# Kernel optimization log

Measured on AMD Instinct MI355X. Metric: run time of the kernel, lower is better.

The kernel has to match this reference:

```python
import jax, jax.numpy as jnp
import numpy as np

B, N, L = 32, 1024, 128
K, D_E, H = 3, 16, 4


def setup_inputs() -> dict:
    key = jax.random.key(0)
    ks = jax.random.split(key, 7)
    return {
        "x": jax.random.normal(ks[0], (B, N, L), jnp.float32),
        # mild scaling on embeddings/projections keeps softmax logits in a sane range
        "psi_emb": jax.random.normal(ks[1], (N, D_E), jnp.float32) * 0.3,
        "psi": jnp.float32(1.0),
        "W_q": jax.random.normal(ks[2], (D_E, H, D_E), jnp.float32) * 0.2,
        "W_k": jax.random.normal(ks[3], (D_E, H, D_E), jnp.float32) * 0.2,
        "attn_alpha": jnp.float32(0.5),
        "F_w": jax.random.normal(ks[4], (H, D_E, K + 1, L), jnp.float32) * 0.1,
        "f_b": jax.random.normal(ks[5], (H, D_E), jnp.float32),
        "head_mix": jnp.ones((H,), jnp.float32),
    }


def reference(x, psi_emb, psi, W_q, W_k, attn_alpha, F_w, f_b, head_mix):
    # x: (B, N, L)
    n = x.shape[1]
    # --- gaussian adjacency: softmax over columns of exp(-psi * ||psi_i - psi_j||^2)
    diff = psi_emb[:, None, :] - psi_emb[None, :, :]          # (N, N, d_e)
    dist2 = jnp.sum(diff * diff, axis=-1)                     # (N, N)
    A_base = jax.nn.softmax(jnp.exp(-psi * dist2), axis=1)    # (N, N)
    # --- per-head attention adjacency
    Q = jnp.einsum('nd,dhm->nhm', psi_emb, W_q)               # (N, H, d_e)
    Kt = jnp.einsum('nd,dhm->nhm', psi_emb, W_k)              # (N, H, d_e)
    scale = 1.0 / jnp.sqrt(jnp.asarray(Q.shape[-1], x.dtype))
    A_attn = jax.nn.softmax(
        jnp.einsum('nhd,mhd->hnm', Q, Kt) * scale, axis=-1)   # (H, N, N)
    # --- sigmoid blend (all heads at once)
    alpha = jax.nn.sigmoid(attn_alpha)
    A_eff = alpha * A_base[None] + (1.0 - alpha) * A_attn     # (H, N, N)
    # --- Chebyshev recursion: T0 = I, T1 = A, Tk = 2 A T_{k-1} - T_{k-2}
    I = jnp.broadcast_to(jnp.eye(n, dtype=x.dtype), A_eff.shape)
    supports = [I, A_eff]
    for _ in range(2, K + 1):
        supports.append(2.0 * jnp.einsum('hnm,hml->hnl', A_eff, supports[-1]) - supports[-2])
    S = jnp.stack(supports, axis=1)                           # (H, K+1, N, N)
    # --- per-node filters
    W_filter = jnp.einsum('nd,hdkl->hnkl', psi_emb, F_w)      # (H, N, K+1, L)
    b_filter = jnp.einsum('nd,hd->hn', psi_emb, f_b)          # (H, N)
    # --- graph conv + node-specific contraction
    x_g = jnp.einsum('hknm,bml->bhknl', S, x)                 # (B, H, K+1, N, L)
    out_h = jnp.einsum('bhknl,hnkl->bhn', x_g, W_filter) + b_filter[None]
    # --- head mixing
    mix_w = jax.nn.softmax(head_mix, axis=0)                  # (H,)
    return jnp.einsum('bhn,h->bn', out_h, mix_w)              # (B, N)
```

## Files before the change

### kernel.cpp

```cpp
#include <hip/hip_runtime.h>
#include <cstdint>

#define NN 1024
#define BB 32
#define LL 128
#define DE 16
#define HH 4
#define K1 4
#define BD 512
#define NS 524288

using bf16x8 = __attribute__((ext_vector_type(8))) short;
using f32x4  = __attribute__((ext_vector_type(4))) float;
using u16x4  = __attribute__((ext_vector_type(4))) unsigned short;

__device__ inline unsigned short f2bf(float f) {
    unsigned u = __builtin_bit_cast(unsigned, f);
    u += 0x7FFFu + ((u >> 16) & 1u);
    return (unsigned short)(u >> 16);
}
__device__ inline float bf2f(unsigned short u) {
    return __builtin_bit_cast(float, (unsigned)u << 16);
}

typedef const __attribute__((address_space(1))) void gas_void;
typedef __attribute__((address_space(3))) void las_void;
#define GLD16(gsrc, ldst) \
    __builtin_amdgcn_global_load_lds((gas_void*)(gsrc), (las_void*)(ldst), 16, 0, 0)

struct LogitsSmem {
    float ejs[64][17];
    float eis[64][17];
    float kjs[64][64];
    float qis[4][64][17];
    float part[4][5][64];
    float wq[1024];
    float wk[1024];
};
struct XtSmem { float xs[64][128]; };

__global__ __launch_bounds__(256) void phase1(
    const float* __restrict__ psi_emb, const float* __restrict__ psi_p,
    const float* __restrict__ W_q, const float* __restrict__ W_k,
    const float* __restrict__ x, const float* __restrict__ F_w,
    short* __restrict__ bnt, short* __restrict__ ant, float* __restrict__ partials,
    short* __restrict__ xt, short* __restrict__ wtt, float* __restrict__ out)
{
    __shared__ __align__(16) char smem_raw[sizeof(LogitsSmem)];
    const int bid = blockIdx.x;
    const int tid = threadIdx.x;

    if (bid < 256) {
        LogitsSmem& S = *(LogitsSmem*)smem_raw;
        const int jb = bid & 15, ib = bid >> 4;
        const int i0 = ib * 64, j0 = jb * 64;
        {
            const int row = tid >> 2, dq = (tid & 3) * 4;
            const float4 vj = *(const float4*)(psi_emb + (j0 + row) * DE + dq);
            S.ejs[row][dq] = vj.x; S.ejs[row][dq + 1] = vj.y;
            S.ejs[row][dq + 2] = vj.z; S.ejs[row][dq + 3] = vj.w;
            const float4 vi = *(const float4*)(psi_emb + (i0 + row) * DE + dq);
            S.eis[row][dq] = vi.x; S.eis[row][dq + 1] = vi.y;
            S.eis[row][dq + 2] = vi.z; S.eis[row][dq + 3] = vi.w;
            *(float4*)&S.wq[tid * 4] = *(const float4*)(W_q + tid * 4);
            *(float4*)&S.wk[tid * 4] = *(const float4*)(W_k + tid * 4);
        }
        __syncthreads();
#pragma unroll
        for (int rep = 0; rep < 16; rep++) {
            const int idx = rep * 256 + tid;
            const int row = idx >> 6, hm = idx & 63;
            float qv = 0.f, kv = 0.f;
#pragma unroll
            for (int d = 0; d < DE; d++) {
                qv += S.eis[row][d] * S.wq[d * 64 + hm];
                kv += S.ejs[row][d] * S.wk[d * 64 + hm];
            }
            S.qis[hm >> 4][row][hm & 15] = qv;
            S.kjs[row][hm] = kv;
        }
        __syncthreads();

        const int i = tid & 63, jg = tid >> 6;
        const float psi = psi_p[0];
        float er[DE];
#pragma unroll
        for (int d = 0; d < DE; d++) er[d] = S.eis[i][d];

        float sb = 0.f, sa[HH] = {0.f, 0.f, 0.f, 0.f};
#pragma unroll
        for (int g = 0; g < 2; g++) {
            unsigned short bw[8];
#pragma unroll
            for (int r = 0; r < 8; r++) {
                const int j = jg * 16 + g * 8 + r;
                float d2 = 0.f;
#pragma unroll
                for (int d = 0; d < DE; d++) { const float t = er[d] - S.ejs[j][d]; d2 += t * t; }
                const float bn = __expf(__expf(-psi * d2));
                sb += bn;
                bw[r] = f2bf(bn);
            }
            uint4 pk;
            pk.x = bw[0] | ((unsigned)bw[1] << 16);
            pk.y = bw[2] | ((unsigned)bw[3] << 16);
            pk.z = bw[4] | ((unsigned)bw[5] << 16);
            pk.w = bw[6] | ((unsigned)bw[7] << 16);
            const size_t toff = (size_t)((j0 + jg * 16 + g * 8) >> 3) * 8192 + (size_t)(i0 + i) * 8;
            *(uint4*)(bnt + toff) = pk;
        }
#pragma unroll
        for (int h = 0; h < HH; h++) {
            float qr[DE];
#pragma unroll
            for (int m = 0; m < DE; m++) qr[m] = S.qis[h][i][m];
#pragma unroll
            for (int g = 0; g < 2; g++) {
                unsigned short aw[8];
#pragma unroll
                for (int r = 0; r < 8; r++) {
                    const int j = jg * 16 + g * 8 + r;
                    float dot = 0.f;
#pragma unroll
                    for (int m = 0; m < DE; m++) dot += qr[m] * S.kjs[j][h * DE + m];
                    const float an = __expf(dot * 0.25f);
                    sa[h] += an;
                    aw[r] = f2bf(an);
                }
                uint4 pk;
                pk.x = aw[0] | ((unsigned)aw[1] << 16);
                pk.y = aw[2] | ((unsigned)aw[3] << 16);
                pk.z = aw[4] | ((unsigned)aw[5] << 16);
                pk.w = aw[6] | ((unsigned)aw[7] << 16);
                const size_t toff = (size_t)((j0 + jg * 16 + g * 8) >> 3) * 8192 + (size_t)(i0 + i) * 8;
                *(uint4*)(ant + (size_t)h * 1048576 + toff) = pk;
            }
        }
        S.part[jg][0][i] = sb;
#pragma unroll
        for (int h = 0; h < HH; h++) S.part[jg][1 + h][i] = sa[h];
        __syncthreads();
        if (tid < 64) {
#pragma unroll
            for (int s = 0; s < 5; s++) {
                const float v = S.part[0][s][tid] + S.part[1][s][tid] +
                                S.part[2][s][tid] + S.part[3][s][tid];
                partials[(size_t)jb * 5120 + (size_t)s * 1024 + i0 + tid] = v;
            }
        }
    } else if (bid < 768) {
        XtSmem& X = *(XtSmem*)smem_raw;
        const int idx = bid - 256;
        const int m0 = (idx & 15) * 64;
        const int b  = idx >> 4;
        for (int i = tid; i < 2048; i += 256) {
            const int row = i >> 5, lq = i & 31;
            *(float4*)&X.xs[row][lq * 4] =
                *(const float4*)(x + ((size_t)(b * NN + m0 + row)) * LL + lq * 4);
        }
        __syncthreads();
        for (int j = tid; j < 1024; j += 256) {
            const int m = j & 63, lc = j >> 6;
            const float* s = &X.xs[m][lc * 8];
            uint4 pk;
            pk.x = f2bf(s[0]) | ((unsigned)f2bf(s[1]) << 16);
            pk.y = f2bf(s[2]) | ((unsigned)f2bf(s[3]) << 16);
            pk.z = f2bf(s[4]) | ((unsigned)f2bf(s[5]) << 16);
            pk.w = f2bf(s[6]) | ((unsigned)f2bf(s[7]) << 16);
            *(uint4*)(xt + (size_t)b * 131072 + (size_t)lc * 8192 + (size_t)(m0 + m) * 8) = pk;
        }
    } else if (bid < 784) {
        const int j = (bid - 768) * 256 + tid;
        const int lc = j >> 8, c = j & 255;
        const int h = c >> 6, k = (c >> 4) & 3, d = c & 15;
        const float* s = F_w + (size_t)((h * DE + d) * K1 + k) * LL + lc * 8;
        uint4 pk;
        pk.x = f2bf(s[0]) | ((unsigned)f2bf(s[1]) << 16);
        pk.y = f2bf(s[2]) | ((unsigned)f2bf(s[3]) << 16);
        pk.z = f2bf(s[4]) | ((unsigned)f2bf(s[5]) << 16);
        pk.w = f2bf(s[6]) | ((unsigned)f2bf(s[7]) << 16);
        *(uint4*)(wtt + (size_t)lc * 2048 + (size_t)c * 8) = pk;
    } else {
        const int idx = (bid - 784) * 256 + tid;
        const float4 z = {0.f, 0.f, 0.f, 0.f};
        *(float4*)(out + (size_t)idx * 8) = z;
        *(float4*)(out + (size_t)idx * 8 + 4) = z;
    }
}

__global__ __launch_bounds__(256) void phase2(
    const short* __restrict__ xt, const short* __restrict__ wtt,
    short* __restrict__ Gt,
    const short* __restrict__ bnt, const short* __restrict__ ant,
    const float* __restrict__ partials, const float* __restrict__ alpha_p,
    short* __restrict__ At)
{
    const int bid = blockIdx.x;
    const int tid = threadIdx.x;
    __shared__ float sums_l[5][64];

    if (bid < 1024) {
        const int cb = bid & 3;
        const int m0 = ((bid >> 2) & 15) * 64;
        const int bp = bid >> 6;
        const int wave = tid >> 6, lane = tid & 63;
        const int b  = bp * 2 + (wave >> 1);
        const int wc = wave & 1;
        const int q = lane >> 4, m16 = lane & 15;
        const short* xb = xt + (size_t)b * 131072;

        f32x4 acc[4][2];
#pragma unroll
        for (int mi = 0; mi < 4; mi++)
#pragma unroll
            for (int ni = 0; ni < 2; ni++) acc[mi][ni] = (f32x4){0.f, 0.f, 0.f, 0.f};

#pragma unroll
        for (int ks = 0; ks < 4; ks++) {
            const int kc = ks * 4 + q;
            bf16x8 a[4], bb[2];
#pragma unroll
            for (int mi = 0; mi < 4; mi++)
                a[mi] = *(const bf16x8*)(xb + (size_t)kc * 8192 + (size_t)(m0 + mi * 16 + m16) * 8);
#pragma unroll
            for (int ni = 0; ni < 2; ni++)
                bb[ni] = *(const bf16x8*)(wtt + (size_t)kc * 2048 +
                                          (size_t)(cb * 64 + wc * 32 + ni * 16 + m16) * 8);
#pragma unroll
            for (int mi = 0; mi < 4; mi++)
#pragma unroll
                for (int ni = 0; ni < 2; ni++)
                    acc[mi][ni] = __builtin_amdgcn_mfma_f32_16x16x32_bf16(a[mi], bb[ni], acc[mi][ni], 0, 0, 0);
        }

#pragma unroll
        for (int ni = 0; ni < 2; ni++) {
            const int cc = cb * 64 + wc * 32 + ni * 16 + m16;
            const int kk = (cc >> 4) & 3, hh = cc >> 6;
            const int col512 = b * 16 + (cc & 15);
            short* gdst = Gt + (size_t)(kk * 4 + hh) * 524288;
#pragma unroll
            for (int mi = 0; mi < 4; mi++) {
                const int row0 = m0 + mi * 16 + q * 4;
                ushort4 pk;
                pk.x = f2bf(acc[mi][ni][0]); pk.y = f2bf(acc[mi][ni][1]);
                pk.z = f2bf(acc[mi][ni][2]); pk.w = f2bf(acc[mi][ni][3]);
                *(ushort4*)(gdst + ((size_t)(row0 >> 3) * 512 + col512) * 8 + (row0 & 7)) = pk;
            }
        }
    } else {
        const int idx = bid - 1024;
        const int jb = idx & 15, ib = idx >> 4;
        const int i0 = ib * 64, j0 = jb * 64;
        const int lane = tid & 63, w = tid >> 6;
        {
            float acc = 0.f;
#pragma unroll
            for (int jb2 = 0; jb2 < 16; jb2++)
                acc += partials[(size_t)jb2 * 5120 + (size_t)w * 1024 + i0 + lane];
            sums_l[w][lane] = acc;
            if (w == 0) {
                float a4 = 0.f;
#pragma unroll
                for (int jb2 = 0; jb2 < 16; jb2++)
                    a4 += partials[(size_t)jb2 * 5120 + 4 * 1024 + i0 + lane];
                sums_l[4][lane] = a4;
            }
        }
        __syncthreads();
        const int i = lane, jg = w;
        const float alpha = 1.f / (1.f + __expf(-alpha_p[0]));
        const float ibs = alpha / sums_l[0][i];
        float ias[HH];
#pragma unroll
        for (int h = 0; h < HH; h++) ias[h] = (1.f - alpha) / sums_l[1 + h][i];

#pragma unroll
        for (int g = 0; g < 2; g++) {
            const size_t toff = (size_t)((j0 + jg * 16 + g * 8) >> 3) * 8192 + (size_t)(i0 + i) * 8;
            const uint4 bp = *(const uint4*)(bnt + toff);
            float bnv[8];
            bnv[0] = bf2f(bp.x & 0xFFFF); bnv[1] = bf2f(bp.x >> 16);
            bnv[2] = bf2f(bp.y & 0xFFFF); bnv[3] = bf2f(bp.y >> 16);
            bnv[4] = bf2f(bp.z & 0xFFFF); bnv[5] = bf2f(bp.z >> 16);
            bnv[6] = bf2f(bp.w & 0xFFFF); bnv[7] = bf2f(bp.w >> 16);
#pragma unroll
            for (int h = 0; h < HH; h++) {
                const uint4 ap = *(const uint4*)(ant + (size_t)h * 1048576 + toff);
                float av[8];
                av[0] = bf2f(ap.x & 0xFFFF); av[1] = bf2f(ap.x >> 16);
                av[2] = bf2f(ap.y & 0xFFFF); av[3] = bf2f(ap.y >> 16);
                av[4] = bf2f(ap.z & 0xFFFF); av[5] = bf2f(ap.z >> 16);
                av[6] = bf2f(ap.w & 0xFFFF); av[7] = bf2f(ap.w >> 16);
                unsigned short ow[8];
#pragma unroll
                for (int r = 0; r < 8; r++) ow[r] = f2bf(ibs * bnv[r] + ias[h] * av[r]);
                uint4 pk;
                pk.x = ow[0] | ((unsigned)ow[1] << 16);
                pk.y = ow[2] | ((unsigned)ow[3] << 16);
                pk.z = ow[4] | ((unsigned)ow[5] << 16);
                pk.w = ow[6] | ((unsigned)ow[7] << 16);
                *(uint4*)(At + (size_t)h * 1048576 + toff) = pk;
            }
        }
    }
}

__global__ __launch_bounds__(256) void gemm_mf(
    const short* __restrict__ At, const short* __restrict__ Bt,
    const short* __restrict__ Pt, const short* __restrict__ Qt,
    short* __restrict__ Ot, float scale, float pc, float qc)
{
    const int bid = blockIdx.x;
    const int h = (bid & 7) >> 1;
    const int tile = ((bid >> 3) << 1) | (bid & 1);
    const int c0 = (tile & 7) * 64;
    const int r0 = (tile >> 3) * 64;

    const short* Ah = At + (size_t)h * 1048576;
    const short* Bh = Bt + (size_t)h * 524288;
    const short* Ph = Pt + (size_t)h * 524288;
    const short* Qh = Qt + (size_t)h * 524288;
    short* Oh = Ot + (size_t)h * 524288;

    const int tid = threadIdx.x;
    const int wave = tid >> 6, lane = tid & 63;
    const int q = lane >> 4, m16 = lane & 15;
    const int wr = wave >> 1, wc = wave & 1;

    __shared__ __align__(16) short Asm[4][4][64][8];
    __shared__ __align__(16) short Bsm[4][4][64][8];

    const char* Abase = (const char*)Ah + (size_t)r0 * 16;
    const char* Bbase = (const char*)Bh + (size_t)c0 * 16;

#define STAGE_MF(itc, bufc)                                                     \
    do {                                                                        \
        const size_t ko_ = (size_t)((itc) * 4 + wave);                          \
        GLD16(Abase + ko_ * 16384 + (size_t)lane * 16, &Asm[bufc][wave][0][0]); \
        GLD16(Bbase + ko_ * 8192  + (size_t)lane * 16, &Bsm[bufc][wave][0][0]); \
    } while (0)

    f32x4 acc[2][2];
#pragma unroll
    for (int mi = 0; mi < 2; mi++)
#pragma unroll
        for (int ni = 0; ni < 2; ni++) acc[mi][ni] = (f32x4){0.f, 0.f, 0.f, 0.f};

    STAGE_MF(0, 0);
    STAGE_MF(1, 1);
    STAGE_MF(2, 2);

#pragma unroll
    for (int it = 0; it < 32; ++it) {
        if (it < 29) STAGE_MF(it + 3, (it + 3) & 3);
        if (it < 29)      asm volatile("s_waitcnt vmcnt(6)" ::: "memory");
        else if (it == 29) asm volatile("s_waitcnt vmcnt(4)" ::: "memory");
        else if (it == 30) asm volatile("s_waitcnt vmcnt(2)" ::: "memory");
        else               asm volatile("s_waitcnt vmcnt(0)" ::: "memory");
        __builtin_amdgcn_s_barrier();

        const int b = it & 3;
        const bf16x8 af0 = *(const bf16x8*)&Asm[b][q][wr * 32 + m16][0];
        const bf16x8 af1 = *(const bf16x8*)&Asm[b][q][wr * 32 + 16 + m16][0];
        const bf16x8 bf0 = *(const bf16x8*)&Bsm[b][q][wc * 32 + m16][0];
        const bf16x8 bf1 = *(const bf16x8*)&Bsm[b][q][wc * 32 + 16 + m16][0];
        acc[0][0] = __builtin_amdgcn_mfma_f32_16x16x32_bf16(af0, bf0, acc[0][0], 0, 0, 0);
        acc[0][1] = __builtin_amdgcn_mfma_f32_16x16x32_bf16(af0, bf1, acc[0][1], 0, 0, 0);
        acc[1][0] = __builtin_amdgcn_mfma_f32_16x16x32_bf16(af1, bf0, acc[1][0], 0, 0, 0);
        acc[1][1] = __builtin_amdgcn_mfma_f32_16x16x32_bf16(af1, bf1, acc[1][1], 0, 0, 0);

        __builtin_amdgcn_s_barrier();
    }
#undef STAGE_MF

#pragma unroll
    for (int mi = 0; mi < 2; mi++) {
        const int row0 = r0 + wr * 32 + mi * 16 + q * 4;
#pragma unroll
        for (int ni = 0; ni < 2; ni++) {
            const int cc = c0 + wc * 32 + ni * 16 + m16;
            const size_t off = ((size_t)(row0 >> 3) * 512 + cc) * 8 + (row0 & 7);
            const u16x4 pv = __builtin_nontemporal_load((const u16x4*)(Ph + off));
            float v[4];
            v[0] = scale * acc[mi][ni][0] + pc * bf2f(pv[0]);
            v[1] = scale * acc[mi][ni][1] + pc * bf2f(pv[1]);
            v[2] = scale * acc[mi][ni][2] + pc * bf2f(pv[2]);
            v[3] = scale * acc[mi][ni][3] + pc * bf2f(pv[3]);
            if (qc != 0.f) {
                const u16x4 qv = __builtin_nontemporal_load((const u16x4*)(Qh + off));
                v[0] += qc * bf2f(qv[0]); v[1] += qc * bf2f(qv[1]);
                v[2] += qc * bf2f(qv[2]); v[3] += qc * bf2f(qv[3]);
            }
            ushort4 pk;
            pk.x = f2bf(v[0]); pk.y = f2bf(v[1]); pk.z = f2bf(v[2]); pk.w = f2bf(v[3]);
            *(ushort4*)(Oh + off) = pk;
        }
    }
}

__global__ __launch_bounds__(256) void gemm3_out(
    const short* __restrict__ At, const short* __restrict__ Bt,
    const short* __restrict__ Pt, const short* __restrict__ Qt,
    const float* __restrict__ psi_emb, const float* __restrict__ f_b,
    const float* __restrict__ head_mix, float* __restrict__ out)
{
    const int bid = blockIdx.x;
    const int h = (bid & 7) >> 1;
    const int tile = ((bid >> 3) << 1) | (bid & 1);
    const int c0 = (tile & 7) * 64;
    const int r0 = (tile >> 3) * 64;

    const short* Ah = At + (size_t)h * 1048576;
    const short* Bh = Bt + (size_t)h * 524288;
    const short* Ph = Pt + (size_t)h * 524288;
    const short* Qh = Qt + (size_t)h * 524288;

    const int tid = threadIdx.x;
    const int wave = tid >> 6, lane = tid & 63;
    const int q = lane >> 4, m16 = lane & 15;
    const int wr = wave >> 1, wc = wave & 1;

    __shared__ float es[64][17];
    __shared__ __align__(16) short Asm[4][4][64][8];
    __shared__ __align__(16) short Bsm[4][4][64][8];

    {
        const int row = tid >> 2, dq = (tid & 3) * 4;
        const float4 ev = *(const float4*)(psi_emb + (size_t)(r0 + row) * DE + dq);
        es[row][dq] = ev.x; es[row][dq + 1] = ev.y;
        es[row][dq + 2] = ev.z; es[row][dq + 3] = ev.w;
    }
    __syncthreads();

    const char* Abase = (const char*)Ah + (size_t)r0 * 16;
    const char* Bbase = (const char*)Bh + (size_t)c0 * 16;

#define STAGE_G3(itc, bufc)                                                     \
    do {                                                                        \
        const size_t ko_ = (size_t)((itc) * 4 + wave);                          \
        GLD16(Abase + ko_ * 16384 + (size_t)lane * 16, &Asm[bufc][wave][0][0]); \
        GLD16(Bbase + ko_ * 8192  + (size_t)lane * 16, &Bsm[bufc][wave][0][0]); \
    } while (0)

    f32x4 acc[2][2];
#pragma unroll
    for (int mi = 0; mi < 2; mi++)
#pragma unroll
        for (int ni = 0; ni < 2; ni++) acc[mi][ni] = (f32x4){0.f, 0.f, 0.f, 0.f};

    STAGE_G3(0, 0);
    STAGE_G3(1, 1);
    STAGE_G3(2, 2);

#pragma unroll
    for (int it = 0; it < 32; ++it) {
        if (it < 29) STAGE_G3(it + 3, (it + 3) & 3);
        if (it < 29)      asm volatile("s_waitcnt vmcnt(6)" ::: "memory");
        else if (it == 29) asm volatile("s_waitcnt vmcnt(4)" ::: "memory");
        else if (it == 30) asm volatile("s_waitcnt vmcnt(2)" ::: "memory");
        else               asm volatile("s_waitcnt vmcnt(0)" ::: "memory");
        __builtin_amdgcn_s_barrier();

        const int b = it & 3;
        const bf16x8 af0 = *(const bf16x8*)&Asm[b][q][wr * 32 + m16][0];
        const bf16x8 af1 = *(const bf16x8*)&Asm[b][q][wr * 32 + 16 + m16][0];
        const bf16x8 bf0 = *(const bf16x8*)&Bsm[b][q][wc * 32 + m16][0];
        const bf16x8 bf1 = *(const bf16x8*)&Bsm[b][q][wc * 32 + 16 + m16][0];
        acc[0][0] = __builtin_amdgcn_mfma_f32_16x16x32_bf16(af0, bf0, acc[0][0], 0, 0, 0);
        acc[0][1] = __builtin_amdgcn_mfma_f32_16x16x32_bf16(af0, bf1, acc[0][1], 0, 0, 0);
        acc[1][0] = __builtin_amdgcn_mfma_f32_16x16x32_bf16(af1, bf0, acc[1][0], 0, 0, 0);
        acc[1][1] = __builtin_amdgcn_mfma_f32_16x16x32_bf16(af1, bf1, acc[1][1], 0, 0, 0);

        __builtin_amdgcn_s_barrier();
    }
#undef STAGE_G3

    const float hm0 = head_mix[0], hm1 = head_mix[1], hm2 = head_mix[2], hm3 = head_mix[3];
    const float mx = fmaxf(fmaxf(hm0, hm1), fmaxf(hm2, hm3));
    const float w0 = expf(hm0 - mx), w1 = expf(hm1 - mx), w2 = expf(hm2 - mx), w3 = expf(hm3 - mx);
    const float isum = 1.f / (w0 + w1 + w2 + w3);
    const float mwh = (h == 0 ? w0 : h == 1 ? w1 : h == 2 ? w2 : w3) * isum;
    const float fb = f_b[h * DE + m16];

#pragma unroll
    for (int mi = 0; mi < 2; mi++) {
        const int rloc0 = wr * 32 + mi * 16 + q * 4;
        const int row0 = r0 + rloc0;
#pragma unroll
        for (int ni = 0; ni < 2; ni++) {
            const int cc = c0 + wc * 32 + ni * 16 + m16;
            const int b = cc >> 4;
            const size_t off = ((size_t)(row0 >> 3) * 512 + cc) * 8 + (row0 & 7);
            const u16x4 pv = __builtin_nontemporal_load((const u16x4*)(Ph + off));
            const u16x4 qv = __builtin_nontemporal_load((const u16x4*)(Qh + off));
            float v[4];
            v[0] = acc[mi][ni][0] + bf2f(pv[0]) - bf2f(qv[0]);
            v[1] = acc[mi][ni][1] + bf2f(pv[1]) - bf2f(qv[1]);
            v[2] = acc[mi][ni][2] + bf2f(pv[2]) - bf2f(qv[2]);
            v[3] = acc[mi][ni][3] + bf2f(pv[3]) - bf2f(qv[3]);
#pragma unroll
            for (int r = 0; r < 4; r++) {
                float w = es[rloc0 + r][m16] * (v[r] + fb);
                w += __shfl_xor(w, 1, 64);
                w += __shfl_xor(w, 2, 64);
                w += __shfl_xor(w, 4, 64);
                w += __shfl_xor(w, 8, 64);
                if (m16 == 0)
                    atomicAdd(out + (size_t)b * NN + (row0 + r), mwh * w);
            }
        }
    }
}

extern "C" void kernel_launch(void* const* d_in, const int* in_sizes, int n_in,
                              void* d_out, int out_size, void* d_ws, size_t ws_size,
                              hipStream_t stream)
{
    const float* x          = (const float*)d_in[0];
    const float* psi_emb    = (const float*)d_in[1];
    const float* psi        = (const float*)d_in[2];
    const float* W_q        = (const float*)d_in[3];
    const float* W_k        = (const float*)d_in[4];
    const float* attn_alpha = (const float*)d_in[5];
    const float* F_w        = (const float*)d_in[6];
    const float* f_b        = (const float*)d_in[7];
    const float* head_mix   = (const float*)d_in[8];
    float* out = (float*)d_out;

    short* At  = (short*)d_ws;
    short* xt  = At + 4194304;
    short* wtt = xt + 4194304;
    short* Gt  = wtt + 32768;
    short* b2t = Gt + 8388608;
    short* b1t = b2t + 2097152;
    short* bnt = b1t + 2097152;
    short* ant = bnt + 1048576;
    float* partials = (float*)(ant + 4194304);

    const size_t need_bytes =
        (size_t)(4194304 + 4194304 + 32768 + 8388608 + 2097152 + 2097152 + 1048576 + 4194304) * 2 +
        (size_t)81920 * 4;
    if (ws_size < need_bytes) return;

    phase1<<<800, 256, 0, stream>>>(psi_emb, psi, W_q, W_k, x, F_w,
                                    bnt, ant, partials, xt, wtt, out);
    phase2<<<1280, 256, 0, stream>>>(xt, wtt, Gt, bnt, ant, partials,
                                     attn_alpha, At);

    gemm_mf<<<512, 256, 0, stream>>>(At, Gt + 12 * (size_t)524288, Gt + 8 * (size_t)524288,
                                     Gt , b2t, 2.f, 1.f, 0.f);
    gemm_mf<<<512, 256, 0, stream>>>(At, b2t, Gt + 4 * (size_t)524288,
                                     Gt + 12 * (size_t)524288, b1t, 2.f, 1.f, -1.f);
    gemm3_out<<<512, 256, 0, stream>>>(At, b1t, Gt, b2t, psi_emb, f_b, head_mix, out);
}
```

Before: 150.5 us.

## Compute adjacency logits with bf16 MFMA using hi/lo split precision

Replaces the scalar FP32 loops for pairwise squared distances and Q·K attention logits in the logits blocks with 16x16x32 bf16 MFMA instructions. Inputs are split into high and low bf16 parts so the products keep close to FP32 accuracy, and distances are rebuilt as |i|^2+|j|^2-2<i,j>. Row sums are reduced with cross-lane shuffles. The aim is to cut ALU time in the adjacency-building phase, at the cost of some precision risk in the distance expansion and a dropped low×low term.

```diff
diff --git a/kernel.cpp b/kernel.cpp
--- a/kernel.cpp
+++ b/kernel.cpp
@@ -22,6 +22,10 @@
 __device__ inline float bf2f(unsigned short u) {
     return __builtin_bit_cast(float, (unsigned)u << 16);
 }
+__device__ inline ushort4 pk4(unsigned short a, unsigned short b,
+                              unsigned short c, unsigned short d) {
+    ushort4 t; t.x = a; t.y = b; t.z = c; t.w = d; return t;
+}
 
 typedef const __attribute__((address_space(1))) void gas_void;
 typedef __attribute__((address_space(3))) void las_void;
@@ -29,13 +33,16 @@
     __builtin_amdgcn_global_load_lds((gas_void*)(gsrc), (las_void*)(ldst), 16, 0, 0)
 
 struct LogitsSmem {
-    float ejs[64][17];
-    float eis[64][17];
-    float kjs[64][64];
-    float qis[4][64][17];
+    float wqs[1024];
+    float wks[1024];
+    short EAj[64][56];
+    short EBi[64][56];
+    short KAj[64][136];
+    short QBi[64][136];
+    float nis[64];
+    float njs[64];
     float part[4][5][64];
-    float wq[1024];
-    float wk[1024];
+    short zblk[8];
 };
 struct XtSmem { float xs[64][128]; };
 
@@ -54,91 +61,156 @@
         LogitsSmem& S = *(LogitsSmem*)smem_raw;
         const int jb = bid & 15, ib = bid >> 4;
         const int i0 = ib * 64, j0 = jb * 64;
+
+        *(float4*)&S.wqs[tid * 4] = *(const float4*)(W_q + tid * 4);
+        *(float4*)&S.wks[tid * 4] = *(const float4*)(W_k + tid * 4);
+        if (tid == 0) {
+            const bf16x8 z = {0, 0, 0, 0, 0, 0, 0, 0};
+            *(bf16x8*)&S.zblk[0] = z;
+        }
+        __syncthreads();
+
         {
-            const int row = tid >> 2, dq = (tid & 3) * 4;
-            const float4 vj = *(const float4*)(psi_emb + (j0 + row) * DE + dq);
-            S.ejs[row][dq] = vj.x; S.ejs[row][dq + 1] = vj.y;
-            S.ejs[row][dq + 2] = vj.z; S.ejs[row][dq + 3] = vj.w;
-            const float4 vi = *(const float4*)(psi_emb + (i0 + row) * DE + dq);
-            S.eis[row][dq] = vi.x; S.eis[row][dq + 1] = vi.y;
-            S.eis[row][dq + 2] = vi.z; S.eis[row][dq + 3] = vi.w;
-            *(float4*)&S.wq[tid * 4] = *(const float4*)(W_q + tid * 4);
-            *(float4*)&S.wk[tid * 4] = *(const float4*)(W_k + tid * 4);
+            const int prow = tid >> 2, ph = tid & 3;
+            float ei[DE], ej[DE];
+            {
+                const float* pei = psi_emb + (size_t)(i0 + prow) * DE;
+                const float* pej = psi_emb + (size_t)(j0 + prow) * DE;
+#pragma unroll
+                for (int c = 0; c < 4; c++) {
+                    const float4 vi = *(const float4*)(pei + c * 4);
+                    ei[c * 4] = vi.x; ei[c * 4 + 1] = vi.y;
+                    ei[c * 4 + 2] = vi.z; ei[c * 4 + 3] = vi.w;
+                    const float4 vj = *(const float4*)(pej + c * 4);
+                    ej[c * 4] = vj.x; ej[c * 4 + 1] = vj.y;
+                    ej[c * 4 + 2] = vj.z; ej[c * 4 + 3] = vj.w;
+                }
+            }
+            float qv[16], kv[16];
+#pragma unroll
+            for (int m = 0; m < 16; m++) { qv[m] = 0.f; kv[m] = 0.f; }
+#pragma unroll
+            for (int d = 0; d < DE; d++) {
+                const float eid = ei[d], ejd = ej[d];
+#pragma unroll
+                for (int m = 0; m < 16; m++) {
+                    qv[m] += eid * S.wqs[d * 64 + ph * 16 + m];
+                    kv[m] += ejd * S.wks[d * 64 + ph * 16 + m];
+                }
+            }
+            unsigned short qh[16], ql[16], kh[16], kl[16];
+#pragma unroll
+            for (int m = 0; m < 16; m++) {
+                qh[m] = f2bf(qv[m]); ql[m] = f2bf(qv[m] - bf2f(qh[m]));
+                kh[m] = f2bf(kv[m]); kl[m] = f2bf(kv[m] - bf2f(kh[m]));
+            }
+#pragma unroll
+            for (int c = 0; c < 4; c++) {
+                *(ushort4*)&S.QBi[prow][ph * 32 + c * 4] =
+                    pk4(qh[c * 4], qh[c * 4 + 1], qh[c * 4 + 2], qh[c * 4 + 3]);
+                *(ushort4*)&S.QBi[prow][ph * 32 + 16 + c * 4] =
+                    pk4(ql[c * 4], ql[c * 4 + 1], ql[c * 4 + 2], ql[c * 4 + 3]);
+                *(ushort4*)&S.KAj[prow][ph * 32 + c * 4] =
+                    pk4(kh[c * 4], kh[c * 4 + 1], kh[c * 4 + 2], kh[c * 4 + 3]);
+                *(ushort4*)&S.KAj[prow][ph * 32 + 16 + c * 4] =
+                    pk4(kl[c * 4], kl[c * 4 + 1], kl[c * 4 + 2], kl[c * 4 + 3]);
+            }
+            if (ph == 0) {
+                float ni = 0.f, nj = 0.f;
+#pragma unroll
+                for (int d = 0; d < DE; d++) { ni += ei[d] * ei[d]; nj += ej[d] * ej[d]; }
+                S.nis[prow] = ni; S.njs[prow] = nj;
+                unsigned short ih[16], il[16], jh[16], jl[16];
+#pragma unroll
+                for (int d = 0; d < DE; d++) {
+                    ih[d] = f2bf(ei[d]); il[d] = f2bf(ei[d] - bf2f(ih[d]));
+                    jh[d] = f2bf(ej[d]); jl[d] = f2bf(ej[d] - bf2f(jh[d]));
+                }
+#pragma unroll
+                for (int c = 0; c < 4; c++) {
+                    *(ushort4*)&S.EBi[prow][c * 4] =
+                        pk4(ih[c * 4], ih[c * 4 + 1], ih[c * 4 + 2], ih[c * 4 + 3]);
+                    *(ushort4*)&S.EBi[prow][16 + c * 4] =
+                        pk4(il[c * 4], il[c * 4 + 1], il[c * 4 + 2], il[c * 4 + 3]);
+                    *(ushort4*)&S.EAj[prow][c * 4] =
+                        pk4(jh[c * 4], jh[c * 4 + 1], jh[c * 4 + 2], jh[c * 4 + 3]);
+                    *(ushort4*)&S.EAj[prow][16 + c * 4] =
+                        pk4(jl[c * 4], jl[c * 4 + 1], jl[c * 4 + 2], jl[c * 4 + 3]);
+                }
+            }
         }
         __syncthreads();
-#pragma unroll
-        for (int rep = 0; rep < 16; rep++) {
-            const int idx = rep * 256 + tid;
-            const int row = idx >> 6, hm = idx & 63;
-            float qv = 0.f, kv = 0.f;
-#pragma unroll
-            for (int d = 0; d < DE; d++) {
-                qv += S.eis[row][d] * S.wq[d * 64 + hm];
-                kv += S.ejs[row][d] * S.wk[d * 64 + hm];
-            }
-            S.qis[hm >> 4][row][hm & 15] = qv;
-            S.kjs[row][hm] = kv;
-        }
-        __syncthreads();
-
-        const int i = tid & 63, jg = tid >> 6;
+
+        const int w = tid >> 6, lane = tid & 63;
+        const int q = lane >> 4, m16 = lane & 15;
         const float psi = psi_p[0];
-        float er[DE];
-#pragma unroll
-        for (int d = 0; d < DE; d++) er[d] = S.eis[i][d];
-
-        float sb = 0.f, sa[HH] = {0.f, 0.f, 0.f, 0.f};
-#pragma unroll
-        for (int g = 0; g < 2; g++) {
-            unsigned short bw[8];
-#pragma unroll
-            for (int r = 0; r < 8; r++) {
-                const int j = jg * 16 + g * 8 + r;
-                float d2 = 0.f;
-#pragma unroll
-                for (int d = 0; d < DE; d++) { const float t = er[d] - S.ejs[j][d]; d2 += t * t; }
-                const float bn = __expf(__expf(-psi * d2));
-                sb += bn;
-                bw[r] = f2bf(bn);
-            }
-            uint4 pk;
-            pk.x = bw[0] | ((unsigned)bw[1] << 16);
-            pk.y = bw[2] | ((unsigned)bw[3] << 16);
-            pk.z = bw[4] | ((unsigned)bw[5] << 16);
-            pk.w = bw[6] | ((unsigned)bw[7] << 16);
-            const size_t toff = (size_t)((j0 + jg * 16 + g * 8) >> 3) * 8192 + (size_t)(i0 + i) * 8;
-            *(uint4*)(bnt + toff) = pk;
+        const short* zb = &S.zblk[0];
+
+        {
+            const bf16x8 aB = *(const bf16x8*)&S.EAj[w * 16 + m16][q * 8];
+            f32x4 acc[4];
+#pragma unroll
+            for (int ct = 0; ct < 4; ct++) acc[ct] = (f32x4){0.f, 0.f, 0.f, 0.f};
+#pragma unroll
+            for (int ct = 0; ct < 4; ct++) {
+                const short* bc = &S.EBi[ct * 16 + m16][0];
+                const bf16x8 b1 = *(const bf16x8*)(bc + (q & 1) * 8);
+                const bf16x8 b2 = *(const bf16x8*)(q < 2 ? bc + 16 + q * 8 : zb);
+                acc[ct] = __builtin_amdgcn_mfma_f32_16x16x32_bf16(aB, b1, acc[ct], 0, 0, 0);
+                acc[ct] = __builtin_amdgcn_mfma_f32_16x16x32_bf16(aB, b2, acc[ct], 0, 0, 0);
+            }
+            float njr[4];
+#pragma unroll
+            for (int r = 0; r < 4; r++) njr[r] = S.njs[w * 16 + q * 4 + r];
+            const size_t tbase = (size_t)((j0 + w * 16 + q * 4) >> 3) * 8192 + (q & 1) * 4;
+#pragma unroll
+            for (int ct = 0; ct < 4; ct++) {
+                const float nii = S.nis[ct * 16 + m16];
+                float s = 0.f; unsigned short pw[4];
+#pragma unroll
+                for (int r = 0; r < 4; r++) {
+                    const float d2 = nii + njr[r] - 2.f * acc[ct][r];
+                    const float bn = __expf(__expf(-psi * d2));
+                    s += bn; pw[r] = f2bf(bn);
+                }
+                *(ushort4*)(bnt + tbase + (size_t)(i0 + ct * 16 + m16) * 8) =
+                    pk4(pw[0], pw[1], pw[2], pw[3]);
+                s += __shfl_xor(s, 16, 64);
+                s += __shfl_xor(s, 32, 64);
+                if (q == 0) S.part[w][0][ct * 16 + m16] = s;
+            }
         }
 #pragma unroll
         for (int h = 0; h < HH; h++) {
-            float qr[DE];
-#pragma unroll
-            for (int m = 0; m < DE; m++) qr[m] = S.qis[h][i][m];
-#pragma unroll
-            for (int g = 0; g < 2; g++) {
-                unsigned short aw[8];
-#pragma unroll
-                for (int r = 0; r < 8; r++) {
-                    const int j = jg * 16 + g * 8 + r;
-                    float dot = 0.f;
-#pragma unroll
-                    for (int m = 0; m < DE; m++) dot += qr[m] * S.kjs[j][h * DE + m];
-                    const float an = __expf(dot * 0.25f);
-                    sa[h] += an;
-                    aw[r] = f2bf(an);
+            const bf16x8 aK = *(const bf16x8*)&S.KAj[w * 16 + m16][h * 32 + q * 8];
+            f32x4 acc[4];
+#pragma unroll
+            for (int ct = 0; ct < 4; ct++) acc[ct] = (f32x4){0.f, 0.f, 0.f, 0.f};
+#pragma unroll
+            for (int ct = 0; ct < 4; ct++) {
+                const short* qc = &S.QBi[ct * 16 + m16][h * 32];
+                const bf16x8 b1 = *(const bf16x8*)(qc + (q & 1) * 8);
+                const bf16x8 b2 = *(const bf16x8*)(q < 2 ? qc + 16 + q * 8 : zb);
+                acc[ct] = __builtin_amdgcn_mfma_f32_16x16x32_bf16(aK, b1, acc[ct], 0, 0, 0);
+                acc[ct] = __builtin_amdgcn_mfma_f32_16x16x32_bf16(aK, b2, acc[ct], 0, 0, 0);
+            }
+            const size_t tbase = (size_t)((j0 + w * 16 + q * 4) >> 3) * 8192 + (q & 1) * 4;
+#pragma unroll
+            for (int ct = 0; ct < 4; ct++) {
+                float s = 0.f; unsigned short pw[4];
+#pragma unroll
+                for (int r = 0; r < 4; r++) {
+                    const float an = __expf(acc[ct][r] * 0.25f);
+                    s += an; pw[r] = f2bf(an);
                 }
-                uint4 pk;
-                pk.x = aw[0] | ((unsigned)aw[1] << 16);
-                pk.y = aw[2] | ((unsigned)aw[3] << 16);
-                pk.z = aw[4] | ((unsigned)aw[5] << 16);
-                pk.w = aw[6] | ((unsigned)aw[7] << 16);
-                const size_t toff = (size_t)((j0 + jg * 16 + g * 8) >> 3) * 8192 + (size_t)(i0 + i) * 8;
-                *(uint4*)(ant + (size_t)h * 1048576 + toff) = pk;
-            }
-        }
-        S.part[jg][0][i] = sb;
-#pragma unroll
-        for (int h = 0; h < HH; h++) S.part[jg][1 + h][i] = sa[h];
+                *(ushort4*)(ant + (size_t)h * 1048576 + tbase +
+                            (size_t)(i0 + ct * 16 + m16) * 8) =
+                    pk4(pw[0], pw[1], pw[2], pw[3]);
+                s += __shfl_xor(s, 16, 64);
+                s += __shfl_xor(s, 32, 64);
+                if (q == 0) S.part[w][1 + h][ct * 16 + m16] = s;
+            }
+        }
         __syncthreads();
         if (tid < 64) {
 #pragma unroll
```

Result: no change. 150.2 us (median of 2 runs) (-0.2%).
